# Kernel tuning notes

Measured on AMD Instinct MI355X. Metric: run time of the kernel, lower is better.

Reference implementation:

```python
import jax, jax.numpy as jnp
import numpy as np

B, N, C, H = 4, 2048, 1024, 16
D = C // H
SCALE = D ** -0.5


def setup_inputs() -> dict:
    key = jax.random.key(0)
    k1, k2, k3 = jax.random.split(key, 3)
    x = jax.random.normal(k1, (B, N, C), dtype=jnp.float32)
    w_qkv = jax.random.normal(k2, (C, 3 * C), dtype=jnp.float32) * (C ** -0.5)
    w_proj = jax.random.normal(k3, (C, C), dtype=jnp.float32) * (C ** -0.5)
    b_proj = jnp.zeros((C,), dtype=jnp.float32)
    return {"x": x, "w_qkv": w_qkv, "w_proj": w_proj, "b_proj": b_proj}


def reference(x, w_qkv, w_proj, b_proj):
    # qkv projection (no bias): [B,N,3C] -> [3,B,H,N,D]
    qkv = (x @ w_qkv).reshape(B, N, 3, H, D).transpose(2, 0, 3, 1, 4)
    q, k, v = qkv[0], qkv[1], qkv[2]
    # scores [B,H,N,N]
    attn = jax.nn.softmax(jnp.einsum('bhnd,bhmd->bhnm', q, k) * SCALE, axis=-1)
    out = jnp.einsum('bhnm,bhmd->bhnd', attn, v)          # [B,H,N,D]
    out = out.transpose(0, 2, 1, 3).reshape(B, N, C)       # [B,N,C]
    return out @ w_proj + b_proj
```

## Files before the change

kernel.cpp:

```cpp
#include <hip/hip_runtime.h>
#include <hip/hip_bf16.h>
#include <cstdint>
#include <cstddef>

typedef unsigned int uint;
typedef unsigned short ushort;

constexpr int Bn = 4, Nn = 2048, Cc = 1024, Hh = 16;
constexpr int ROWS = Bn * Nn;
constexpr int QKVC = 3 * Cc;
constexpr float SL2 = 0.18033688011118f;

typedef __bf16 bf16_t;
typedef bf16_t bf16x8 __attribute__((ext_vector_type(8)));
typedef float f32x4 __attribute__((ext_vector_type(4)));

__device__ __forceinline__ ushort f2bf(float f) {
  union { __bf16 b; ushort u; } cv;
  cv.b = (__bf16)f;
  return cv.u;
}
__device__ __forceinline__ float exp2v(float x) { return __builtin_exp2f(x); }

__device__ __forceinline__ void gload_lds16(const void* g, void* l) {
  __builtin_amdgcn_global_load_lds(
      (const __attribute__((address_space(1))) void*)g,
      (__attribute__((address_space(3))) void*)l, 16, 0, 0);
}

__global__ __launch_bounds__(256) void cvt_bf16_kernel(
    const float* __restrict__ in, ushort* __restrict__ out) {
  int i = blockIdx.x * 256 + threadIdx.x;
  const float4* ip = (const float4*)in;
  float4 a = ip[i * 2], b = ip[i * 2 + 1];
  uint4 w;
  w.x = (uint)f2bf(a.x) | ((uint)f2bf(a.y) << 16);
  w.y = (uint)f2bf(a.z) | ((uint)f2bf(a.w) << 16);
  w.z = (uint)f2bf(b.x) | ((uint)f2bf(b.y) << 16);
  w.w = (uint)f2bf(b.z) | ((uint)f2bf(b.w) << 16);
  ((uint4*)out)[i] = w;
}

__global__ __launch_bounds__(256) void transpose_cvt_kernel(
    const float* __restrict__ W, ushort* __restrict__ Wt, int K, int N) {
  __shared__ float tile[64][65];
  const int n0 = blockIdx.x * 64, k0 = blockIdx.y * 64;
  const int tid = threadIdx.x;
#pragma unroll
  for (int it = 0; it < 16; it++) {
    int idx = tid + it * 256;
    int r = idx >> 6, c = idx & 63;
    tile[r][c] = W[(size_t)(k0 + r) * N + n0 + c];
  }
  __syncthreads();
#pragma unroll
  for (int it = 0; it < 16; it++) {
    int idx = tid + it * 256;
    int r = idx >> 6, c = idx & 63;
    Wt[(size_t)(n0 + r) * K + k0 + c] = f2bf(tile[c][r]);
  }
}

template <int MODE>
__global__ __launch_bounds__(256) void gemm128_kernel(
    const ushort* __restrict__ A, const ushort* __restrict__ Bt,
    void* __restrict__ Cout, void* __restrict__ Vout,
    const float* __restrict__ bias, int M, int N, int K) {
  __shared__ ushort As[128 * 32];
  __shared__ ushort Bs[128 * 32];
  const int tid = threadIdx.x;
  const int lane = tid & 63;
  const int wid = tid >> 6;
  const int wm = wid >> 1, wn = wid & 1;
  const int l16 = lane & 15, g = lane >> 4;
  const int n0 = blockIdx.x * 128, m0 = blockIdx.y * 128;

  const int c0 = tid, c1 = tid + 256;
  const ushort* Ab = A + (size_t)m0 * K;
  const ushort* Bb = Bt + (size_t)n0 * K;
  f32x4 acc[4][4] = {};

  for (int k0 = 0; k0 < K; k0 += 32) {
    gload_lds16(Ab + (size_t)(c0 >> 2) * K + k0 + (c0 & 3) * 8, As + c0 * 8);
    gload_lds16(Ab + (size_t)(c1 >> 2) * K + k0 + (c1 & 3) * 8, As + c1 * 8);
    gload_lds16(Bb + (size_t)(c0 >> 2) * K + k0 + (c0 & 3) * 8, Bs + c0 * 8);
    gload_lds16(Bb + (size_t)(c1 >> 2) * K + k0 + (c1 & 3) * 8, Bs + c1 * 8);
    __syncthreads();
    bf16x8 af[4], bfr[4];
#pragma unroll
    for (int mf = 0; mf < 4; mf++)
      af[mf] = *(const bf16x8*)(As + (wm * 64 + mf * 16 + l16) * 32 + g * 8);
#pragma unroll
    for (int nf = 0; nf < 4; nf++)
      bfr[nf] = *(const bf16x8*)(Bs + (wn * 64 + nf * 16 + l16) * 32 + g * 8);
#pragma unroll
    for (int mf = 0; mf < 4; mf++)
#pragma unroll
      for (int nf = 0; nf < 4; nf++)
        acc[mf][nf] = __builtin_amdgcn_mfma_f32_16x16x32_bf16(af[mf], bfr[nf], acc[mf][nf], 0, 0, 0);
    __syncthreads();
  }

#pragma unroll
  for (int mf = 0; mf < 4; mf++) {
    const int orow0 = m0 + wm * 64 + mf * 16 + g * 4;
#pragma unroll
    for (int nf = 0; nf < 4; nf++) {
      int col = n0 + wn * 64 + nf * 16 + l16;
      if (MODE == 0) {
        if (col < 2048) {
#pragma unroll
          for (int r = 0; r < 4; r++)
            ((ushort*)Cout)[(size_t)(orow0 + r) * 2048 + col] = f2bf(acc[mf][nf][r]);
        } else {
          int hh = (col - 2048) >> 6, dd = (col - 2048) & 63;
          int bb = orow0 >> 11, nn = orow0 & 2047;
          ushort4 w;
          w.x = f2bf(acc[mf][nf][0]); w.y = f2bf(acc[mf][nf][1]);
          w.z = f2bf(acc[mf][nf][2]); w.w = f2bf(acc[mf][nf][3]);
          *(ushort4*)((ushort*)Vout + ((size_t)(bb * 16 + hh) * 64 + dd) * 2048 + nn) = w;
        }
      } else {
#pragma unroll
        for (int r = 0; r < 4; r++)
          ((float*)Cout)[(size_t)(orow0 + r) * N + col] = acc[mf][nf][r] + bias[col];
      }
    }
  }
}

__global__ __launch_bounds__(256, 4) void flash_mfma_kernel(
    const ushort* __restrict__ qk, const ushort* __restrict__ vt,
    ushort* __restrict__ obf) {
  __shared__ ushort Ks[2][64 * 64];
  __shared__ ushort Vs[2][64 * 64];
  const int tid = threadIdx.x;
  const int lane = tid & 63, wid = tid >> 6;
  const int l16 = lane & 15, g = lane >> 4;

  const int f = blockIdx.x + (int)(gridDim.x * blockIdx.y);
  const int xcd = f & 7, slot = f >> 3;
  const int bh = xcd * 8 + (slot >> 4);
  const int qx = slot & 15;
  const int b = bh >> 4, h = bh & 15;
  const int q0 = qx * 128 + wid * 32;

  const int sc0 = tid, sc1 = tid + 256;
  const int sr0 = sc0 >> 3, scol0 = ((sc0 & 7) ^ (sr0 & 7)) * 8;
  const int sr1 = sc1 >> 3, scol1 = ((sc1 & 7) ^ (sr1 & 7)) * 8;
  const ushort* Kbase = qk + (size_t)b * Nn * 2048 + 1024 + h * 64;
  const ushort* Vbase = vt + (size_t)bh * 64 * 2048;

#define STAGE(buf, kv0)                                                       \
  do {                                                                        \
    gload_lds16(Kbase + (size_t)((kv0) + sr0) * 2048 + scol0,                 \
                &Ks[buf][0] + sc0 * 8);                                       \
    gload_lds16(Kbase + (size_t)((kv0) + sr1) * 2048 + scol1,                 \
                &Ks[buf][0] + sc1 * 8);                                       \
    gload_lds16(Vbase + (size_t)sr0 * 2048 + (kv0) + scol0,                   \
                &Vs[buf][0] + sc0 * 8);                                       \
    gload_lds16(Vbase + (size_t)sr1 * 2048 + (kv0) + scol1,                   \
                &Vs[buf][0] + sc1 * 8);                                       \
  } while (0)

  bf16x8 qf[2][2];
#pragma unroll
  for (int qh = 0; qh < 2; qh++)
#pragma unroll
    for (int kc = 0; kc < 2; kc++)
      qf[qh][kc] = *(const bf16x8*)(
          qk + (size_t)(b * Nn + q0 + qh * 16 + l16) * 2048 + h * 64 + kc * 32 + g * 8);

  union { ushort us[8]; bf16x8 v; } onesu;
#pragma unroll
  for (int j = 0; j < 8; j++) onesu.us[j] = 0x3F80;
  const bf16x8 ones = onesu.v;

  f32x4 oacc[2][4] = {};
  f32x4 lacc[2] = {};
  float mrun[2] = {-INFINITY, -INFINITY};

  STAGE(0, 0);

  for (int t = 0; t < Nn / 64; ++t) {
    const int cur = t & 1;
    asm volatile("s_waitcnt vmcnt(0)" ::: "memory");
    __builtin_amdgcn_s_barrier();
    asm volatile("" ::: "memory");
    if (t < Nn / 64 - 1) STAGE(cur ^ 1, (t + 1) * 64);

    const ushort* Kc = &Ks[cur][0];
    const ushort* Vc = &Vs[cur][0];

    f32x4 sacc[2][4] = {};
    __builtin_amdgcn_s_setprio(1);
#pragma unroll
    for (int kc = 0; kc < 2; kc++) {
#pragma unroll
      for (int jc = 0; jc < 4; jc++) {
        int row = jc * 16 + l16;
        bf16x8 kf = *(const bf16x8*)(Kc + row * 64 + ((kc * 32 + g * 8) ^ ((row & 7) << 3)));
        sacc[0][jc] = __builtin_amdgcn_mfma_f32_16x16x32_bf16(kf, qf[0][kc], sacc[0][jc], 0, 0, 0);
        sacc[1][jc] = __builtin_amdgcn_mfma_f32_16x16x32_bf16(kf, qf[1][kc], sacc[1][jc], 0, 0, 0);
      }
    }
    __builtin_amdgcn_s_setprio(0);

    float pmax[2];
#pragma unroll
    for (int qh = 0; qh < 2; qh++) {
      float mj0 = fmaxf(fmaxf(fmaxf(sacc[qh][0][0], sacc[qh][0][1]), sacc[qh][0][2]), sacc[qh][0][3]);
      float mj1 = fmaxf(fmaxf(fmaxf(sacc[qh][1][0], sacc[qh][1][1]), sacc[qh][1][2]), sacc[qh][1][3]);
      float mj2 = fmaxf(fmaxf(fmaxf(sacc[qh][2][0], sacc[qh][2][1]), sacc[qh][2][2]), sacc[qh][2][3]);
      float mj3 = fmaxf(fmaxf(fmaxf(sacc[qh][3][0], sacc[qh][3][1]), sacc[qh][3][2]), sacc[qh][3][3]);
      float mx = fmaxf(fmaxf(fmaxf(mj0, mj1), mj2), mj3);
      mx = fmaxf(mx, __shfl_xor(mx, 16));
      mx = fmaxf(mx, __shfl_xor(mx, 32));
      pmax[qh] = mx * SL2;
    }
    bool need = (pmax[0] > mrun[0] + 8.f) || (pmax[1] > mrun[1] + 8.f);
    if (__any(need)) {
#pragma unroll
      for (int qh = 0; qh < 2; qh++) {
        float mnew = fmaxf(mrun[qh], pmax[qh]);
        float alpha = exp2v(mrun[qh] - mnew);
        mrun[qh] = mnew;
#pragma unroll
        for (int r = 0; r < 4; r++) {
          float ar = __shfl(alpha, g * 4 + r);
#pragma unroll
          for (int dc = 0; dc < 4; dc++) oacc[qh][dc][r] *= ar;
          lacc[qh][r] *= ar;
        }
      }
    }

    bf16x8 pa[2][2];
#pragma unroll
    for (int qh = 0; qh < 2; qh++) {
      uint pk_[4][2];
#pragma unroll
      for (int jc = 0; jc < 4; jc++) {
        float p0 = exp2v(fmaf(sacc[qh][jc][0], SL2, -mrun[qh]));
        float p1 = exp2v(fmaf(sacc[qh][jc][1], SL2, -mrun[qh]));
        float p2 = exp2v(fmaf(sacc[qh][jc][2], SL2, -mrun[qh]));
        float p3 = exp2v(fmaf(sacc[qh][jc][3], SL2, -mrun[qh]));
        asm("v_cvt_pk_bf16_f32 %0, %1, %2" : "=v"(pk_[jc][0]) : "v"(p0), "v"(p1));
        asm("v_cvt_pk_bf16_f32 %0, %1, %2" : "=v"(pk_[jc][1]) : "v"(p2), "v"(p3));
      }
#pragma unroll
      for (int kc = 0; kc < 2; kc++) {
        uint a0 = pk_[kc * 2][0], b0 = pk_[kc * 2 + 1][0];
        asm("v_permlane32_swap_b32 %0, %1" : "+v"(a0), "+v"(b0));
        asm("v_permlane16_swap_b32 %0, %1" : "+v"(a0), "+v"(b0));
        uint a1 = pk_[kc * 2][1], b1 = pk_[kc * 2 + 1][1];
        asm("v_permlane32_swap_b32 %0, %1" : "+v"(a1), "+v"(b1));
        asm("v_permlane16_swap_b32 %0, %1" : "+v"(a1), "+v"(b1));
        union { uint4 u; bf16x8 v; } cv;
        cv.u.x = a0; cv.u.y = a1; cv.u.z = b0; cv.u.w = b1;
        pa[qh][kc] = cv.v;
      }
    }

    __builtin_amdgcn_s_setprio(1);
#pragma unroll
    for (int kc = 0; kc < 2; kc++) {
#pragma unroll
      for (int dc = 0; dc < 4; dc++) {
        int row = dc * 16 + l16;
        bf16x8 vf = *(const bf16x8*)(Vc + row * 64 + ((kc * 32 + g * 8) ^ ((row & 7) << 3)));
        oacc[0][dc] = __builtin_amdgcn_mfma_f32_16x16x32_bf16(pa[0][kc], vf, oacc[0][dc], 0, 0, 0);
        oacc[1][dc] = __builtin_amdgcn_mfma_f32_16x16x32_bf16(pa[1][kc], vf, oacc[1][dc], 0, 0, 0);
      }
      lacc[0] = __builtin_amdgcn_mfma_f32_16x16x32_bf16(pa[0][kc], ones, lacc[0], 0, 0, 0);
      lacc[1] = __builtin_amdgcn_mfma_f32_16x16x32_bf16(pa[1][kc], ones, lacc[1], 0, 0, 0);
    }
    __builtin_amdgcn_s_setprio(0);
  }
#undef STAGE

#pragma unroll
  for (int qh = 0; qh < 2; qh++) {
    f32x4 linv;
#pragma unroll
    for (int r = 0; r < 4; r++) linv[r] = 1.f / lacc[qh][r];
#pragma unroll
    for (int r = 0; r < 4; r++) {
      int grow = b * Nn + q0 + qh * 16 + g * 4 + r;
      ushort* op = obf + (size_t)grow * Cc + h * 64 + l16;
#pragma unroll
      for (int dc = 0; dc < 4; dc++)
        op[dc * 16] = f2bf(oacc[qh][dc][r] * linv[r]);
    }
  }
}

extern "C" void kernel_launch(void* const* d_in, const int* in_sizes, int n_in,
                              void* d_out, int out_size, void* d_ws, size_t ws_size,
                              hipStream_t stream) {
  const float* x      = (const float*)d_in[0];
  const float* w_qkv  = (const float*)d_in[1];
  const float* w_proj = (const float*)d_in[2];
  const float* b_proj = (const float*)d_in[3];
  float* out = (float*)d_out;

  char* ws = (char*)d_ws;
  ushort* Xbf    = (ushort*)(ws);
  ushort* WqkvT  = (ushort*)(ws + (16u << 20));
  ushort* WprojT = (ushort*)(ws + (22u << 20));
  ushort* QKbf   = (ushort*)(ws + (24u << 20));
  ushort* Vtg    = (ushort*)(ws + (56u << 20));
  ushort* Obf    = (ushort*)(ws + (72u << 20));

  cvt_bf16_kernel<<<4096, 256, 0, stream>>>(x, Xbf);
  transpose_cvt_kernel<<<dim3(QKVC / 64, Cc / 64), 256, 0, stream>>>(w_qkv, WqkvT, Cc, QKVC);
  transpose_cvt_kernel<<<dim3(Cc / 64, Cc / 64), 256, 0, stream>>>(w_proj, WprojT, Cc, Cc);
  gemm128_kernel<0><<<dim3(QKVC / 128, ROWS / 128), 256, 0, stream>>>(
      Xbf, WqkvT, QKbf, Vtg, nullptr, ROWS, QKVC, Cc);
  flash_mfma_kernel<<<dim3(Nn / 128, Bn * Hh), 256, 0, stream>>>(QKbf, Vtg, Obf);
  gemm128_kernel<1><<<dim3(Cc / 128, ROWS / 128), 256, 0, stream>>>(
      Obf, WprojT, out, nullptr, b_proj, ROWS, Cc, Cc);
}
```

Baseline: 239.2 us.

## Software-pipeline QK of next tile with PV and fold softmax scale into Q

```diff
diff --git a/kernel.cpp b/kernel.cpp
--- a/kernel.cpp
+++ b/kernel.cpp
@@ -109,9 +109,10 @@
       int col = n0 + wn * 64 + nf * 16 + l16;
       if (MODE == 0) {
         if (col < 2048) {
+          const float qs = (col < 1024) ? SL2 : 1.0f;
 #pragma unroll
           for (int r = 0; r < 4; r++)
-            ((ushort*)Cout)[(size_t)(orow0 + r) * 2048 + col] = f2bf(acc[mf][nf][r]);
+            ((ushort*)Cout)[(size_t)(orow0 + r) * 2048 + col] = f2bf(acc[mf][nf][r] * qs);
         } else {
           int hh = (col - 2048) >> 6, dd = (col - 2048) & 63;
           int bb = orow0 >> 11, nn = orow0 & 2047;
@@ -133,7 +134,7 @@
     const ushort* __restrict__ qk, const ushort* __restrict__ vt,
     ushort* __restrict__ obf) {
   __shared__ ushort Ks[2][64 * 64];
-  __shared__ ushort Vs[2][64 * 64];
+  __shared__ ushort Vs[3][64 * 64];
   const int tid = threadIdx.x;
   const int lane = tid & 63, wid = tid >> 6;
   const int l16 = lane & 15, g = lane >> 4;
@@ -151,12 +152,15 @@
   const ushort* Kbase = qk + (size_t)b * Nn * 2048 + 1024 + h * 64;
   const ushort* Vbase = vt + (size_t)bh * 64 * 2048;
 
-#define STAGE(buf, kv0)                                                       \
+#define KSTAGE(buf, kv0)                                                      \
   do {                                                                        \
     gload_lds16(Kbase + (size_t)((kv0) + sr0) * 2048 + scol0,                 \
                 &Ks[buf][0] + sc0 * 8);                                       \
     gload_lds16(Kbase + (size_t)((kv0) + sr1) * 2048 + scol1,                 \
                 &Ks[buf][0] + sc1 * 8);                                       \
+  } while (0)
+#define VSTAGE(buf, kv0)                                                      \
+  do {                                                                        \
     gload_lds16(Vbase + (size_t)sr0 * 2048 + (kv0) + scol0,                   \
                 &Vs[buf][0] + sc0 * 8);                                       \
     gload_lds16(Vbase + (size_t)sr1 * 2048 + (kv0) + scol1,                   \
@@ -179,33 +183,37 @@
   f32x4 oacc[2][4] = {};
   f32x4 lacc[2] = {};
   float mrun[2] = {-INFINITY, -INFINITY};
-
-  STAGE(0, 0);
-
-  for (int t = 0; t < Nn / 64; ++t) {
-    const int cur = t & 1;
-    asm volatile("s_waitcnt vmcnt(0)" ::: "memory");
-    __builtin_amdgcn_s_barrier();
-    asm volatile("" ::: "memory");
-    if (t < Nn / 64 - 1) STAGE(cur ^ 1, (t + 1) * 64);
-
-    const ushort* Kc = &Ks[cur][0];
-    const ushort* Vc = &Vs[cur][0];
-
-    f32x4 sacc[2][4] = {};
-    __builtin_amdgcn_s_setprio(1);
-#pragma unroll
-    for (int kc = 0; kc < 2; kc++) {
+  f32x4 sacc[2][4];
+
+  auto qk_compute = [&](const ushort* Kc) {
+#pragma unroll
+    for (int qh = 0; qh < 2; qh++)
+#pragma unroll
+      for (int jc = 0; jc < 4; jc++)
+        sacc[qh][jc] = f32x4{0.f, 0.f, 0.f, 0.f};
+#pragma unroll
+    for (int kc = 0; kc < 2; kc++)
 #pragma unroll
       for (int jc = 0; jc < 4; jc++) {
-        int row = jc * 16 + l16;
+        const int row = jc * 16 + l16;
         bf16x8 kf = *(const bf16x8*)(Kc + row * 64 + ((kc * 32 + g * 8) ^ ((row & 7) << 3)));
         sacc[0][jc] = __builtin_amdgcn_mfma_f32_16x16x32_bf16(kf, qf[0][kc], sacc[0][jc], 0, 0, 0);
         sacc[1][jc] = __builtin_amdgcn_mfma_f32_16x16x32_bf16(kf, qf[1][kc], sacc[1][jc], 0, 0, 0);
       }
-    }
-    __builtin_amdgcn_s_setprio(0);
-
+  };
+
+  constexpr int NT = Nn / 64;
+  KSTAGE(0, 0); VSTAGE(0, 0);
+  KSTAGE(1, 64); VSTAGE(1, 64);
+  asm volatile("s_waitcnt vmcnt(4)" ::: "memory");
+  __builtin_amdgcn_s_barrier();
+  asm volatile("" ::: "memory");
+  __builtin_amdgcn_s_setprio(1);
+  qk_compute(&Ks[0][0]);
+  __builtin_amdgcn_s_setprio(0);
+
+  int vcur = 0;
+  for (int t = 0; t < NT; ++t) {
     float pmax[2];
 #pragma unroll
     for (int qh = 0; qh < 2; qh++) {
@@ -216,7 +224,7 @@
       float mx = fmaxf(fmaxf(fmaxf(mj0, mj1), mj2), mj3);
       mx = fmaxf(mx, __shfl_xor(mx, 16));
       mx = fmaxf(mx, __shfl_xor(mx, 32));
-      pmax[qh] = mx * SL2;
+      pmax[qh] = mx;
     }
     bool need = (pmax[0] > mrun[0] + 8.f) || (pmax[1] > mrun[1] + 8.f);
     if (__any(need)) {
@@ -241,10 +249,10 @@
       uint pk_[4][2];
 #pragma unroll
       for (int jc = 0; jc < 4; jc++) {
-        float p0 = exp2v(fmaf(sacc[qh][jc][0], SL2, -mrun[qh]));
-        float p1 = exp2v(fmaf(sacc[qh][jc][1], SL2, -mrun[qh]));
-        float p2 = exp2v(fmaf(sacc[qh][jc][2], SL2, -mrun[qh]));
-        float p3 = exp2v(fmaf(sacc[qh][jc][3], SL2, -mrun[qh]));
+        float p0 = exp2v(sacc[qh][jc][0] - mrun[qh]);
+        float p1 = exp2v(sacc[qh][jc][1] - mrun[qh]);
+        float p2 = exp2v(sacc[qh][jc][2] - mrun[qh]);
+        float p3 = exp2v(sacc[qh][jc][3] - mrun[qh]);
         asm("v_cvt_pk_bf16_f32 %0, %1, %2" : "=v"(pk_[jc][0]) : "v"(p0), "v"(p1));
         asm("v_cvt_pk_bf16_f32 %0, %1, %2" : "=v"(pk_[jc][1]) : "v"(p2), "v"(p3));
       }
@@ -262,6 +270,22 @@
       }
     }
 
+    const ushort* Vc = &Vs[vcur][0];
+
+    if (t < NT - 1) {
+      asm volatile("s_waitcnt vmcnt(0)" ::: "memory");
+      __builtin_amdgcn_s_barrier();
+      asm volatile("" ::: "memory");
+      if (t + 2 < NT) {
+        int vst = vcur - 1; if (vst < 0) vst += 3;
+        KSTAGE(t & 1, (t + 2) * 64);
+        VSTAGE(vst, (t + 2) * 64);
+      }
+      __builtin_amdgcn_s_setprio(1);
+      qk_compute(&Ks[(t + 1) & 1][0]);
+      __builtin_amdgcn_s_setprio(0);
+    }
+
     __builtin_amdgcn_s_setprio(1);
 #pragma unroll
     for (int kc = 0; kc < 2; kc++) {
@@ -276,8 +300,11 @@
       lacc[1] = __builtin_amdgcn_mfma_f32_16x16x32_bf16(pa[1][kc], ones, lacc[1], 0, 0, 0);
     }
     __builtin_amdgcn_s_setprio(0);
-  }
-#undef STAGE
+
+    vcur = (vcur == 2) ? 0 : vcur + 1;
+  }
+#undef KSTAGE
+#undef VSTAGE
 
 #pragma unroll
   for (int qh = 0; qh < 2; qh++) {
```

After: 254.0 us. 6.2% more time.
